# Performance work log

Measured on AMD Instinct MI355X. Metric: run time of the kernel, lower is better.

The kernel has to match this reference:

```python
import jax, jax.numpy as jnp
import numpy as np

DIM = 768
N_HEADS = 12
HEAD_DIM = DIM // N_HEADS
SCALE = HEAD_DIM ** -0.5


def setup_inputs() -> dict:
    key = jax.random.key(0)
    ks = jax.random.split(key, 5)
    B, N = 8, 1024
    x = jax.random.normal(ks[0], (B, N, DIM), dtype=jnp.float32)
    # Linear weights stored as (in, out) for x @ W; torch stores (out, in).
    w_qkv = jax.random.normal(ks[1], (DIM, 3 * DIM), dtype=jnp.float32) * (DIM ** -0.5)
    b_qkv = jnp.zeros((3 * DIM,), dtype=jnp.float32)
    w_proj = jax.random.normal(ks[2], (DIM, DIM), dtype=jnp.float32) * (DIM ** -0.5)
    b_proj = jnp.zeros((DIM,), dtype=jnp.float32)
    return {"x": x, "w_qkv": w_qkv, "b_qkv": b_qkv, "w_proj": w_proj, "b_proj": b_proj}


def reference(x, w_qkv, b_qkv, w_proj, b_proj):
    B, N, _ = x.shape
    qkv = x @ w_qkv + b_qkv                       # [B, N, 3*dim]
    qkv = qkv.reshape(B, N, 3, N_HEADS, HEAD_DIM)
    qkv = jnp.transpose(qkv, (2, 0, 3, 1, 4))     # [3, B, H, N, hd]
    q, k, v = qkv[0], qkv[1], qkv[2]
    attn = jnp.einsum("bhqd,bhkd->bhqk", q, k) * SCALE
    attn = jax.nn.softmax(attn, axis=-1)
    out = jnp.einsum("bhqk,bhkd->bhqd", attn, v)  # [B, H, N, hd]
    out = jnp.transpose(out, (0, 2, 1, 3)).reshape(B, N, DIM)
    return out @ w_proj + b_proj
```

## Files before the change

kernel.cpp:

```cpp
#include <hip/hip_runtime.h>
#include <cstdint>

#define DIM 768
#define NH 12
#define HD 64
#define SEQ 1024
#define NBH 96

#define QOFF  ((size_t)0)
#define KOFF  ((size_t)6291456)
#define VOFF  ((size_t)12582912)
#define AOFF  ((size_t)18874368)
#define XOFF  ((size_t)25165824)
#define WQOFF ((size_t)31457280)
#define WPOFF ((size_t)33226752)

#define QSCALE 0.18033688f

#define WAIT_VM8   __builtin_amdgcn_s_waitcnt(0x0F78)
#define WAIT_VM0   __builtin_amdgcn_s_waitcnt(0x0F70)
#define WAIT_LGKM0 __builtin_amdgcn_s_waitcnt(0xC07F)
#define BAR        __builtin_amdgcn_s_barrier()
#define CFENCE     __asm__ __volatile__("" ::: "memory")

typedef __attribute__((ext_vector_type(8))) __bf16 bf16x8;
typedef __attribute__((ext_vector_type(2))) __bf16 bf16x2;
typedef __attribute__((ext_vector_type(4))) float f32x4;
typedef unsigned short u16;

__device__ __forceinline__ u16 f2bf(float f) {
    union { float f; unsigned u; } x; x.f = f;
    unsigned r = x.u + 0x7fffu + ((x.u >> 16) & 1u);
    return (u16)(r >> 16);
}

__device__ __forceinline__ unsigned pkbf(float a, float b) {
#if __has_builtin(__builtin_amdgcn_cvt_pk_bf16_f32)
    bf16x2 v = __builtin_amdgcn_cvt_pk_bf16_f32(a, b);
    union { bf16x2 v; unsigned u; } c; c.v = v; return c.u;
#else
    return (unsigned)f2bf(a) | ((unsigned)f2bf(b) << 16);
#endif
}

__device__ __forceinline__ void async_cp16(const void* g, void* l) {
    __builtin_amdgcn_global_load_lds((const __attribute__((address_space(1))) void*)g,
                                     (__attribute__((address_space(3))) void*)l, 16, 0, 0);
}

__global__ __launch_bounds__(256) void prep(const float* __restrict__ x,
                                            const float* __restrict__ wq,
                                            const float* __restrict__ wp,
                                            u16* __restrict__ ws) {
    const int bid = blockIdx.x;
    const int tid = threadIdx.x;
    if (bid < 6144) {
        int i = bid * 256 + tid;
        float4 v = *(const float4*)&x[(size_t)i * 4];
        ushort4 o; o.x = f2bf(v.x); o.y = f2bf(v.y); o.z = f2bf(v.z); o.w = f2bf(v.w);
        *(ushort4*)&ws[XOFF + (size_t)i * 4] = o;
        return;
    }
    __shared__ float T[64][65];
    const float* w; u16* wt; int N, bx, by;
    if (bid < 6576) { int b = bid - 6144; w = wq; wt = ws + WQOFF; N = 2304; bx = b % 36; by = b / 36; }
    else            { int b = bid - 6576; w = wp; wt = ws + WPOFF; N = 768;  bx = b % 12; by = b / 12; }
    const int K = 768;
    const int k0 = by * 64, n0 = bx * 64;
    const int r = tid >> 4, c4 = (tid & 15) * 4;
#pragma unroll
    for (int i = 0; i < 4; ++i) {
        float4 v = *(const float4*)&w[(size_t)(k0 + r + 16 * i) * N + n0 + c4];
        T[r + 16 * i][c4 + 0] = v.x; T[r + 16 * i][c4 + 1] = v.y;
        T[r + 16 * i][c4 + 2] = v.z; T[r + 16 * i][c4 + 3] = v.w;
    }
    __syncthreads();
#pragma unroll
    for (int i = 0; i < 4; ++i) {
        int rr = r + 16 * i;
        ushort4 o;
        o.x = f2bf(T[c4 + 0][rr]); o.y = f2bf(T[c4 + 1][rr]);
        o.z = f2bf(T[c4 + 2][rr]); o.w = f2bf(T[c4 + 3][rr]);
        *(ushort4*)&wt[(size_t)(n0 + rr) * K + k0 + c4] = o;
    }
}

template <int EPI>
__global__ __launch_bounds__(256) void gemm_bt(const u16* __restrict__ A,
                                               const u16* __restrict__ Bt,
                                               const float* __restrict__ bias,
                                               float* __restrict__ outf,
                                               u16* __restrict__ outq) {
    __shared__ __align__(16) u16 As[2][128 * 64];
    __shared__ __align__(16) u16 Bs[2][128 * 64];
    const int tid = threadIdx.x;
    const int lane = tid & 63;
    const int w = tid >> 6;
    const int wm = w >> 1, wn = w & 1;
    const int m0 = blockIdx.y * 128, n0 = blockIdx.x * 128;

    const int lgrp = lane >> 3;
    const int gg = (lane & 7) ^ lgrp;
    const u16* ga = A  + (size_t)(m0 + w * 32 + lgrp) * 768 + gg * 8;
    const u16* gb = Bt + (size_t)(n0 + w * 32 + lgrp) * 768 + gg * 8;

    const int l15 = lane & 15, qg = lane >> 4, q4 = qg * 4;

    int aoff[4][2], boff[4][2];
#pragma unroll
    for (int r = 0; r < 4; ++r) {
        int row = 64 * wm + 16 * r + l15;
#pragma unroll
        for (int kc = 0; kc < 2; ++kc)
            aoff[r][kc] = row * 64 + (((4 * kc + qg) ^ (row & 7)) << 3);
    }
#pragma unroll
    for (int c = 0; c < 4; ++c) {
        int row = 64 * wn + 16 * c + l15;
#pragma unroll
        for (int kc = 0; kc < 2; ++kc)
            boff[c][kc] = row * 64 + (((4 * kc + qg) ^ (row & 7)) << 3);
    }

#define ISSUE(buf, kk)                                                          \
    {                                                                           \
        _Pragma("unroll")                                                       \
        for (int i = 0; i < 4; ++i) {                                           \
            async_cp16(ga + (size_t)i * 8 * 768 + (kk), &As[buf][w * 2048 + i * 512]); \
            async_cp16(gb + (size_t)i * 8 * 768 + (kk), &Bs[buf][w * 2048 + i * 512]); \
        }                                                                       \
    }

    ISSUE(0, 0)
    ISSUE(1, 64)

    f32x4 acc[4][4] = {};

#pragma unroll
    for (int k = 0; k < 12; ++k) {
        const int cur = k & 1;
        if (k < 11) { WAIT_VM8; } else { WAIT_VM0; }
        BAR;
        CFENCE;
        bf16x8 af[4][2], bfr[4][2];
#pragma unroll
        for (int r = 0; r < 4; ++r)
#pragma unroll
            for (int kc = 0; kc < 2; ++kc) af[r][kc] = *(const bf16x8*)&As[cur][aoff[r][kc]];
#pragma unroll
        for (int c = 0; c < 4; ++c)
#pragma unroll
            for (int kc = 0; kc < 2; ++kc) bfr[c][kc] = *(const bf16x8*)&Bs[cur][boff[c][kc]];
        WAIT_LGKM0;
        CFENCE;
        BAR;
        if (k + 2 < 12) ISSUE(cur, (k + 2) * 64)
#pragma unroll
        for (int kc = 0; kc < 2; ++kc)
#pragma unroll
            for (int r = 0; r < 4; ++r)
#pragma unroll
                for (int c = 0; c < 4; ++c)
                    acc[r][c] = __builtin_amdgcn_mfma_f32_16x16x32_bf16(af[r][kc], bfr[c][kc], acc[r][c], 0, 0, 0);
    }
#undef ISSUE

#pragma unroll
    for (int r = 0; r < 4; ++r) {
#pragma unroll
        for (int c = 0; c < 4; ++c) {
            const int cg = n0 + 64 * wn + 16 * c + l15;
            const float bv = bias[cg];
            const int mb = m0 + 64 * wm + 16 * r + q4;
            if constexpr (EPI == 0) {
#pragma unroll
                for (int g = 0; g < 4; ++g)
                    outf[(size_t)(mb + g) * DIM + cg] = acc[r][c][g] + bv;
            } else {
                const int which = (cg >= 1536) ? 2 : (cg >= 768 ? 1 : 0);
                const int rem = cg - which * 768;
                const int h = rem >> 6, d = rem & 63;
                const int b = mb >> 10, q = mb & 1023;
                if (which == 0) {
#pragma unroll
                    for (int g = 0; g < 4; ++g)
                        outq[QOFF + ((size_t)(b * NH + h) * SEQ + q + g) * HD + d] =
                            f2bf((acc[r][c][g] + bv) * QSCALE);
                } else if (which == 1) {
#pragma unroll
                    for (int g = 0; g < 4; ++g)
                        outq[KOFF + ((size_t)(b * NH + h) * SEQ + q + g) * HD + d] =
                            f2bf(acc[r][c][g] + bv);
                } else {
                    ushort4 pk;
                    pk.x = f2bf(acc[r][c][0] + bv); pk.y = f2bf(acc[r][c][1] + bv);
                    pk.z = f2bf(acc[r][c][2] + bv); pk.w = f2bf(acc[r][c][3] + bv);
                    *(ushort4*)&outq[VOFF + ((size_t)(b * NH + h) * HD + d) * SEQ + q] = pk;
                }
            }
        }
    }
}

__global__ __launch_bounds__(256) void flash_attn(const u16* __restrict__ ws, u16* __restrict__ attn_out) {
    __shared__ __align__(16) u16 Ks[2][64 * 64];
    __shared__ __align__(16) u16 Ps[128 * 64];

    const int tid = threadIdx.x;
    const int lane = tid & 63;
    const int wv = tid >> 6;
    const int qt = blockIdx.x;
    const int bh = blockIdx.y;
    const u16* qp = ws + QOFF + (size_t)bh * SEQ * HD;
    const u16* kp = ws + KOFF + (size_t)bh * SEQ * HD;
    const u16* vp = ws + VOFF + (size_t)bh * HD * SEQ;

    const int l15 = lane & 15, qg = lane >> 4, q8 = qg * 8, q4 = qg * 4;
    const int l7 = l15 & 7;

    bf16x8 bq[2][2];
#pragma unroll
    for (int r = 0; r < 2; ++r)
#pragma unroll
        for (int kc = 0; kc < 2; ++kc)
            bq[r][kc] = *(const bf16x8*)&qp[(size_t)(qt * 128 + 32 * wv + 16 * r + l15) * HD + 32 * kc + q8];

    const int lgrp = lane >> 3;
    const int gg = (lane & 7) ^ lgrp;
    auto kissue = [&](int buf, int ktv) {
#pragma unroll
        for (int i = 0; i < 2; ++i)
            async_cp16(kp + (size_t)(ktv * 64 + wv * 16 + i * 8 + lgrp) * 64 + gg * 8,
                       &Ks[buf][(wv * 16 + i * 8) * 64]);
    };
    kissue(0, 0);

    int akoff[4][2], apoff[2][2], pwoff[2][4];
#pragma unroll
    for (int c = 0; c < 4; ++c)
#pragma unroll
        for (int kc = 0; kc < 2; ++kc)
            akoff[c][kc] = (16 * c + l15) * 64 + (((4 * kc + qg) ^ l7) << 3);
#pragma unroll
    for (int r = 0; r < 2; ++r) {
#pragma unroll
        for (int kc = 0; kc < 2; ++kc)
            apoff[r][kc] = (32 * wv + 16 * r + l15) * 64 + (((4 * kc + qg) ^ l7) << 3);
#pragma unroll
        for (int c = 0; c < 4; ++c)
            pwoff[r][c] = (32 * wv + 16 * r + l15) * 64 + (((2 * c + (qg >> 1)) ^ l7) << 3) + (qg & 1) * 4;
    }

    f32x4 oacc[2][4] = {};
    float lsum[2] = {0.f, 0.f};

    for (int kt = 0; kt < 16; ++kt) {
        const int cur = kt & 1;
        WAIT_VM0;
        BAR;
        CFENCE;

        bf16x8 bv[4][2];
#pragma unroll
        for (int cd = 0; cd < 4; ++cd)
#pragma unroll
            for (int kc = 0; kc < 2; ++kc)
                bv[cd][kc] = *(const bf16x8*)&vp[(size_t)(16 * cd + l15) * SEQ + kt * 64 + 32 * kc + q8];

        f32x4 sacc[4][2] = {};
#pragma unroll
        for (int c = 0; c < 4; ++c) {
#pragma unroll
            for (int kc = 0; kc < 2; ++kc) {
                bf16x8 ak = *(const bf16x8*)&Ks[cur][akoff[c][kc]];
#pragma unroll
                for (int r = 0; r < 2; ++r)
                    sacc[c][r] = __builtin_amdgcn_mfma_f32_16x16x32_bf16(ak, bq[r][kc], sacc[c][r], 0, 0, 0);
            }
        }

#pragma unroll
        for (int r = 0; r < 2; ++r) {
#pragma unroll
            for (int c = 0; c < 4; ++c) {
                float p0 = __builtin_amdgcn_exp2f(sacc[c][r][0]);
                float p1 = __builtin_amdgcn_exp2f(sacc[c][r][1]);
                float p2 = __builtin_amdgcn_exp2f(sacc[c][r][2]);
                float p3 = __builtin_amdgcn_exp2f(sacc[c][r][3]);
                lsum[r] += (p0 + p1) + (p2 + p3);
                uint2 pk2; pk2.x = pkbf(p0, p1); pk2.y = pkbf(p2, p3);
                *(uint2*)&Ps[pwoff[r][c]] = pk2;
            }
        }

        CFENCE;
        WAIT_LGKM0;
        BAR;
        CFENCE;
        if (kt < 15) kissue(cur ^ 1, kt + 1);

#pragma unroll
        for (int r = 0; r < 2; ++r) {
#pragma unroll
            for (int kc = 0; kc < 2; ++kc) {
                bf16x8 ap = *(const bf16x8*)&Ps[apoff[r][kc]];
#pragma unroll
                for (int cd = 0; cd < 4; ++cd)
                    oacc[r][cd] = __builtin_amdgcn_mfma_f32_16x16x32_bf16(ap, bv[cd][kc], oacc[r][cd], 0, 0, 0);
            }
        }
    }

#pragma unroll
    for (int r = 0; r < 2; ++r) {
        lsum[r] += __shfl_xor(lsum[r], 16);
        lsum[r] += __shfl_xor(lsum[r], 32);
    }
    float linv[2][4];
#pragma unroll
    for (int r = 0; r < 2; ++r)
#pragma unroll
        for (int g = 0; g < 4; ++g)
            linv[r][g] = 1.f / __shfl(lsum[r], q4 + g);

    const int b = bh / NH, h = bh % NH;
#pragma unroll
    for (int r = 0; r < 2; ++r) {
#pragma unroll
        for (int g = 0; g < 4; ++g) {
            int qrow = qt * 128 + 32 * wv + 16 * r + q4 + g;
            size_t grow = (size_t)(b * SEQ + qrow) * DIM + h * HD;
#pragma unroll
            for (int cd = 0; cd < 4; ++cd)
                attn_out[grow + 16 * cd + l15] = f2bf(oacc[r][cd][g] * linv[r][g]);
        }
    }
}

extern "C" void kernel_launch(void* const* d_in, const int* in_sizes, int n_in,
                              void* d_out, int out_size, void* d_ws, size_t ws_size,
                              hipStream_t stream) {
    const float* x      = (const float*)d_in[0];
    const float* w_qkv  = (const float*)d_in[1];
    const float* b_qkv  = (const float*)d_in[2];
    const float* w_proj = (const float*)d_in[3];
    const float* b_proj = (const float*)d_in[4];
    float* out = (float*)d_out;
    u16* ws = (u16*)d_ws;

    prep<<<6720, 256, 0, stream>>>(x, w_qkv, w_proj, ws);
    gemm_bt<1><<<dim3(18, 64), 256, 0, stream>>>(ws + XOFF, ws + WQOFF, b_qkv, nullptr, ws);
    flash_attn<<<dim3(8, 96), 256, 0, stream>>>(ws, ws + AOFF);
    gemm_bt<0><<<dim3(6, 64), 256, 0, stream>>>(ws + AOFF, ws + WPOFF, b_proj, out, nullptr);
}
```

Baseline: 218.0 us.

## Keep softmax probabilities in registers and stage V tiles through LDS

The flash attention kernel no longer writes P to shared memory and reads it back. The S accumulator layout is fed directly as the B operand of 16x16x16 bf16 MFMAs, and the PV product is computed transposed (O^T = V^T P^T). V tiles are now double-buffered into LDS with async copies alongside K, replacing per-iteration global loads. This removes one barrier and the P LDS round trip per tile. In exchange the PV product uses a half-depth MFMA with twice as many instructions, and V tiles now add LDS reads. The output store now writes 4-element vectors per lane.

Result: no change. 214.6 us (-1.6%).

```diff
diff --git a/kernel.cpp b/kernel.cpp
--- a/kernel.cpp
+++ b/kernel.cpp
@@ -26,6 +26,7 @@
 typedef __attribute__((ext_vector_type(8))) __bf16 bf16x8;
 typedef __attribute__((ext_vector_type(2))) __bf16 bf16x2;
 typedef __attribute__((ext_vector_type(4))) float f32x4;
+typedef __attribute__((ext_vector_type(4))) short s16x4;
 typedef unsigned short u16;
 
 __device__ __forceinline__ u16 f2bf(float f) {
@@ -204,7 +205,7 @@
 
 __global__ __launch_bounds__(256) void flash_attn(const u16* __restrict__ ws, u16* __restrict__ attn_out) {
     __shared__ __align__(16) u16 Ks[2][64 * 64];
-    __shared__ __align__(16) u16 Ps[128 * 64];
+    __shared__ __align__(16) u16 Vs[2][64 * 64];
 
     const int tid = threadIdx.x;
     const int lane = tid & 63;
@@ -215,7 +216,7 @@
     const u16* kp = ws + KOFF + (size_t)bh * SEQ * HD;
     const u16* vp = ws + VOFF + (size_t)bh * HD * SEQ;
 
-    const int l15 = lane & 15, qg = lane >> 4, q8 = qg * 8, q4 = qg * 4;
+    const int l15 = lane & 15, qg = lane >> 4, q8 = qg * 8;
     const int l7 = l15 & 7;
 
     bf16x8 bq[2][2];
@@ -227,28 +228,26 @@
 
     const int lgrp = lane >> 3;
     const int gg = (lane & 7) ^ lgrp;
-    auto kissue = [&](int buf, int ktv) {
-#pragma unroll
-        for (int i = 0; i < 2; ++i)
+    auto stage = [&](int buf, int ktv) {
+#pragma unroll
+        for (int i = 0; i < 2; ++i) {
             async_cp16(kp + (size_t)(ktv * 64 + wv * 16 + i * 8 + lgrp) * 64 + gg * 8,
                        &Ks[buf][(wv * 16 + i * 8) * 64]);
+            async_cp16(vp + (size_t)(wv * 16 + i * 8 + lgrp) * SEQ + ktv * 64 + gg * 8,
+                       &Vs[buf][(wv * 16 + i * 8) * 64]);
+        }
     };
-    kissue(0, 0);
-
-    int akoff[4][2], apoff[2][2], pwoff[2][4];
-#pragma unroll
-    for (int c = 0; c < 4; ++c)
+    stage(0, 0);
+
+    int akoff[4][2], avoff[4][4];
+#pragma unroll
+    for (int c = 0; c < 4; ++c) {
 #pragma unroll
         for (int kc = 0; kc < 2; ++kc)
             akoff[c][kc] = (16 * c + l15) * 64 + (((4 * kc + qg) ^ l7) << 3);
 #pragma unroll
-    for (int r = 0; r < 2; ++r) {
-#pragma unroll
-        for (int kc = 0; kc < 2; ++kc)
-            apoff[r][kc] = (32 * wv + 16 * r + l15) * 64 + (((4 * kc + qg) ^ l7) << 3);
-#pragma unroll
-        for (int c = 0; c < 4; ++c)
-            pwoff[r][c] = (32 * wv + 16 * r + l15) * 64 + (((2 * c + (qg >> 1)) ^ l7) << 3) + (qg & 1) * 4;
+        for (int cd = 0; cd < 4; ++cd)
+            avoff[c][cd] = (16 * cd + l15) * 64 + (((2 * c + (qg >> 1)) ^ l7) << 3) + (qg & 1) * 4;
     }
 
     f32x4 oacc[2][4] = {};
@@ -259,13 +258,7 @@
         WAIT_VM0;
         BAR;
         CFENCE;
-
-        bf16x8 bv[4][2];
-#pragma unroll
-        for (int cd = 0; cd < 4; ++cd)
-#pragma unroll
-            for (int kc = 0; kc < 2; ++kc)
-                bv[cd][kc] = *(const bf16x8*)&vp[(size_t)(16 * cd + l15) * SEQ + kt * 64 + 32 * kc + q8];
+        if (kt < 15) stage(cur ^ 1, kt + 1);
 
         f32x4 sacc[4][2] = {};
 #pragma unroll
@@ -279,35 +272,33 @@
             }
         }
 
-#pragma unroll
-        for (int r = 0; r < 2; ++r) {
-#pragma unroll
-            for (int c = 0; c < 4; ++c) {
+        s16x4 pf[4][2];
+#pragma unroll
+        for (int c = 0; c < 4; ++c) {
+#pragma unroll
+            for (int r = 0; r < 2; ++r) {
                 float p0 = __builtin_amdgcn_exp2f(sacc[c][r][0]);
                 float p1 = __builtin_amdgcn_exp2f(sacc[c][r][1]);
                 float p2 = __builtin_amdgcn_exp2f(sacc[c][r][2]);
                 float p3 = __builtin_amdgcn_exp2f(sacc[c][r][3]);
                 lsum[r] += (p0 + p1) + (p2 + p3);
-                uint2 pk2; pk2.x = pkbf(p0, p1); pk2.y = pkbf(p2, p3);
-                *(uint2*)&Ps[pwoff[r][c]] = pk2;
+                union { uint2 u; s16x4 v; } pk;
+                pk.u.x = pkbf(p0, p1); pk.u.y = pkbf(p2, p3);
+                pf[c][r] = pk.v;
             }
         }
 
-        CFENCE;
-        WAIT_LGKM0;
-        BAR;
-        CFENCE;
-        if (kt < 15) kissue(cur ^ 1, kt + 1);
-
-#pragma unroll
-        for (int r = 0; r < 2; ++r) {
-#pragma unroll
-            for (int kc = 0; kc < 2; ++kc) {
-                bf16x8 ap = *(const bf16x8*)&Ps[apoff[r][kc]];
+#pragma unroll
+        for (int c = 0; c < 4; ++c) {
+            s16x4 av[4];
+#pragma unroll
+            for (int cd = 0; cd < 4; ++cd)
+                av[cd] = *(const s16x4*)&Vs[cur][avoff[c][cd]];
+#pragma unroll
+            for (int r = 0; r < 2; ++r)
 #pragma unroll
                 for (int cd = 0; cd < 4; ++cd)
-                    oacc[r][cd] = __builtin_amdgcn_mfma_f32_16x16x32_bf16(ap, bv[cd][kc], oacc[r][cd], 0, 0, 0);
-            }
+                    oacc[r][cd] = __builtin_amdgcn_mfma_f32_16x16x16bf16_1k(av[cd], pf[c][r], oacc[r][cd], 0, 0, 0);
         }
     }
 
@@ -316,23 +307,19 @@
         lsum[r] += __shfl_xor(lsum[r], 16);
         lsum[r] += __shfl_xor(lsum[r], 32);
     }
-    float linv[2][4];
-#pragma unroll
-    for (int r = 0; r < 2; ++r)
-#pragma unroll
-        for (int g = 0; g < 4; ++g)
-            linv[r][g] = 1.f / __shfl(lsum[r], q4 + g);
 
     const int b = bh / NH, h = bh % NH;
 #pragma unroll
     for (int r = 0; r < 2; ++r) {
-#pragma unroll
-        for (int g = 0; g < 4; ++g) {
-            int qrow = qt * 128 + 32 * wv + 16 * r + q4 + g;
-            size_t grow = (size_t)(b * SEQ + qrow) * DIM + h * HD;
-#pragma unroll
-            for (int cd = 0; cd < 4; ++cd)
-                attn_out[grow + 16 * cd + l15] = f2bf(oacc[r][cd][g] * linv[r][g]);
+        const float inv = 1.f / lsum[r];
+        const int qrow = qt * 128 + 32 * wv + 16 * r + l15;
+        u16* orow = attn_out + (size_t)(b * SEQ + qrow) * DIM + h * HD + qg * 4;
+#pragma unroll
+        for (int cd = 0; cd < 4; ++cd) {
+            ushort4 o;
+            o.x = f2bf(oacc[r][cd][0] * inv); o.y = f2bf(oacc[r][cd][1] * inv);
+            o.z = f2bf(oacc[r][cd][2] * inv); o.w = f2bf(oacc[r][cd][3] * inv);
+            *(ushort4*)&orow[16 * cd] = o;
         }
     }
 }
```
